# Performance work log

Hardware: AMD Instinct MI355X
Metric: run time of the kernel (lower is better)

Reference implementation:

```python
import jax, jax.numpy as jnp
import numpy as np

R, MAXI, MAXO = 333, 119, 12   # n ROIs, max roi input size, max roi reduced size
E, H = 3328, 8                  # embed dim (concat 3325 + pad 3), heads
HD = E // H                     # 416
CONCAT = 3325
EPS = 1e-5


def _roi_layout():
    """Deterministic synthetic ROI sizes + gather maps for vectorized ragged encode."""
    sizes = 30 + (7 * np.arange(R)) % 90            # per-ROI input widths
    reduced = 8 + np.arange(R) % 5                  # per-ROI output widths
    reduced[332] = 8                                # makes concat+3 divisible by 8
    starts = np.concatenate([[0], np.cumsum(sizes)[:-1]])
    total = int(sizes.sum())                        # 24696
    in_idx = np.minimum(starts[:, None] + np.arange(MAXI)[None, :], total - 1)
    in_mask = (np.arange(MAXI)[None, :] < sizes[:, None]).astype(np.float32)
    out_idx = np.concatenate([i * MAXO + np.arange(reduced[i]) for i in range(R)])
    assert out_idx.shape[0] == CONCAT
    return jnp.asarray(in_idx), jnp.asarray(in_mask), jnp.asarray(out_idx)


def _bn(x, g, b):
    # training-mode BatchNorm1d: biased batch stats (matches torch normalization)
    m = x.mean(0)
    v = x.var(0)
    return (x - m) * jax.lax.rsqrt(v + EPS) * g + b


def _lrelu(x, s):
    return jnp.where(x > 0, x, s * x)


def setup_inputs() -> dict:
    key = jax.random.key(0)
    ks = jax.random.split(key, 16)
    B, TOTAL = 2048, 24696
    f32 = jnp.float32
    return {
        'x': jax.random.normal(ks[0], (B, TOTAL), f32),
        'enc_W': jax.random.normal(ks[1], (R, MAXO, MAXI), f32) * 0.1,
        'enc_b': jax.random.normal(ks[2], (R, MAXO), f32) * 0.02,
        'bn1_g': jnp.ones((CONCAT,), f32),
        'bn1_b': jnp.zeros((CONCAT,), f32),
        'Wqkv': jax.random.normal(ks[3], (3 * E, E), f32) * (1.0 / np.sqrt(E)),
        'bqkv': jnp.zeros((3 * E,), f32),
        'Wo': jax.random.normal(ks[4], (E, E), f32) * (1.0 / np.sqrt(E)),
        'bo': jnp.zeros((E,), f32),
        'W1': jax.random.normal(ks[5], (1024, E), f32) * (1.0 / np.sqrt(E)),
        'b1': jnp.zeros((1024,), f32),
        'bn2_g': jnp.ones((1024,), f32),
        'bn2_b': jnp.zeros((1024,), f32),
        'W2': jax.random.normal(ks[6], (300, 1024), f32) * (1.0 / 32.0),
        'b2': jnp.zeros((300,), f32),
        'Wc': jax.random.normal(ks[7], (180, 300), f32) * 0.06,
        'bc': jnp.zeros((180,), f32),
    }


def reference(x, enc_W, enc_b, bn1_g, bn1_b, Wqkv, bqkv, Wo, bo,
              W1, b1, bn2_g, bn2_b, W2, b2, Wc, bc):
    in_idx, in_mask, out_idx = _roi_layout()
    B = x.shape[0]
    # --- vectorized ragged per-ROI Linear (replaces 333-way python loop) ---
    xp = x[:, in_idx] * in_mask                     # [B, R, MAXI], padded slices
    y = jnp.einsum('bri,roi->bro', xp, enc_W) + enc_b  # [B, R, MAXO]
    y = y.reshape(B, R * MAXO)[:, out_idx]          # ragged concat -> [B, 3325]
    # per-ROI BN+LeakyReLU(0.3) == per-feature on the concat
    y = _lrelu(_bn(y, bn1_g, bn1_b), 0.3)
    y = jnp.pad(y, ((0, 0), (1, 2)))                # F.pad (1, 2) -> [B, 3328]
    # --- MultiheadAttention, seq_len = 1 (input unsqueezed to [1, B, E]) ---
    qkv = y @ Wqkv.T + bqkv                         # [B, 3E]
    q, k, v = jnp.split(qkv, 3, axis=-1)
    q = q.reshape(B, H, 1, HD)
    k = k.reshape(B, H, 1, HD)
    v = v.reshape(B, H, 1, HD)
    s = jnp.einsum('bhqd,bhkd->bhqk', q, k) / jnp.sqrt(jnp.float32(HD))
    a = jax.nn.softmax(s, axis=-1)                  # trivially 1 for L=1, kept faithful
    o = jnp.einsum('bhqk,bhkd->bhqd', a, v).reshape(B, E)
    o = o @ Wo.T + bo
    r = _lrelu(_bn(o @ W1.T + b1, bn2_g, bn2_b), 0.1)
    reg_out = r @ W2.T + b2                         # [B, 300]
    y_pred = jax.nn.softmax(reg_out @ Wc.T + bc, axis=-1)  # [B, 180]
    return reg_out, y_pred
```

## Files before the change

kernel.cpp:

```cpp
#include <hip/hip_runtime.h>
#include <hip/hip_bf16.h>

#define B_      2048
#define R_      333
#define MAXI_   119
#define MAXO_   12
#define CONCAT_ 3325
#define E_      3328
#define TOTAL_  24696
#define HID_    1024
#define NREG_   300
#define NCLS_   180
#define EPS_    1e-5f
#define NSLOT_  128
#define PSTR_   3328
#define NS2_    128

typedef __attribute__((ext_vector_type(8))) short bf16x8;
typedef __attribute__((ext_vector_type(4))) float f32x4;

static __device__ inline unsigned short f2bf_rne(float f) {
  unsigned u;
  __builtin_memcpy(&u, &f, 4);
  u += 0x7fff + ((u >> 16) & 1);
  return (unsigned short)(u >> 16);
}
static __device__ inline float bf2f(unsigned short s) {
  unsigned u = (unsigned)s << 16;
  float f;
  __builtin_memcpy(&f, &u, 4);
  return f;
}

__global__ void layout_kernel(int* __restrict__ starts, int* __restrict__ red_starts) {
  if (threadIdx.x == 0 && blockIdx.x == 0) {
    int s = 0, rs = 0;
    for (int r = 0; r < R_; ++r) {
      starts[r] = s;
      red_starts[r] = rs;
      s += 30 + (7 * r) % 90;
      rs += (r == 332) ? 8 : (8 + r % 5);
    }
  }
}

__global__ __launch_bounds__(256) void prep_cast_kernel(
    const float* __restrict__ W1, unsigned short* __restrict__ W1b,
    const float* __restrict__ W2, unsigned short* __restrict__ W2b) {
  const int n4a = HID_ * E_ / 4, n4b = NREG_ * HID_ / 4;
  int i = blockIdx.x * 256 + threadIdx.x;
  const float* src; unsigned short* dst; int idx;
  if (i < n4a) { src = W1; dst = W1b; idx = i; }
  else if (i < n4a + n4b) { src = W2; dst = W2b; idx = i - n4a; }
  else return;
  float4 v = ((const float4*)src)[idx];
  ushort4 o;
  o.x = f2bf_rne(v.x); o.y = f2bf_rne(v.y); o.z = f2bf_rne(v.z); o.w = f2bf_rne(v.w);
  ((ushort4*)dst)[idx] = o;
}

__device__ __forceinline__ void rowdot_body(
    const float* __restrict__ A, const float* __restrict__ v, const float* __restrict__ b,
    float* __restrict__ out, int N, int K, int jb) {
  int wid = threadIdx.x >> 6, lane = threadIdx.x & 63;
  int j = jb * 4 + wid;
  if (j >= N) return;
  const float* row = A + (size_t)j * K;
  float s = 0.f;
  for (int k = lane; k < K; k += 64) s = fmaf(row[k], v[k], s);
  for (int o = 32; o; o >>= 1) s += __shfl_down(s, o);
  if (lane == 0) out[j] = s + b[j];
}

__global__ __launch_bounds__(256) void trans_rowdot_kernel(
    const float* __restrict__ Wo, const float* __restrict__ Wv,
    unsigned short* __restrict__ WoT, unsigned short* __restrict__ WvT,
    const float* __restrict__ bv, const float* __restrict__ bo, float* __restrict__ t1v) {
  __shared__ float tile[64][65];
  int bid = blockIdx.x;
  const int NT = (E_ / 64) * (E_ / 64);
  if (bid < 2 * NT) {
    int z = bid / NT, rem = bid % NT;
    const float* in = z ? Wv : Wo;
    unsigned short* out = z ? WvT : WoT;
    int c0 = (rem % 52) * 64, r0 = (rem / 52) * 64;
    int t = threadIdx.x;
    int ci = t & 63, ri0 = t >> 6;
    for (int ri = ri0; ri < 64; ri += 4)
      tile[ri][ci] = in[(size_t)(r0 + ri) * E_ + c0 + ci];
    __syncthreads();
    int rj = t & 63, i0 = t >> 6;
    for (int i = i0; i < 64; i += 4)
      out[(size_t)(c0 + i) * E_ + r0 + rj] = f2bf_rne(tile[rj][i]);
  } else {
    rowdot_body(Wo, bv, bo, t1v, E_, E_, bid - 2 * NT);
  }
}

__device__ __forceinline__ void pack_w_body(const float* __restrict__ enc_W,
                                            const int* __restrict__ starts,
                                            unsigned short* __restrict__ Wpk, int r) {
  int tid = threadIdx.x;
  int kc = tid >> 6, lane = tid & 63;
  int size = 30 + (7 * r) % 90;
  int s8 = starts[r] & 7;
  int oc = lane & 15;
  int k0 = kc * 32 + (lane >> 4) * 8;
  unsigned short o[8];
#pragma unroll
  for (int e = 0; e < 8; ++e) {
    int k = k0 + e - s8;
    float v = 0.f;
    if (oc < MAXO_ && k >= 0 && k < size) v = enc_W[((size_t)r * MAXO_ + oc) * MAXI_ + k];
    o[e] = f2bf_rne(v);
  }
  unsigned short* dst = Wpk + ((size_t)r * 4 + kc) * 512 + lane * 8;
  *(ushort4*)dst = *(ushort4*)&o[0];
  *(ushort4*)(dst + 4) = *(ushort4*)&o[4];
}

__global__ __launch_bounds__(256) void packw_rowdot_kernel(
    const float* __restrict__ enc_W, const int* __restrict__ starts,
    unsigned short* __restrict__ Wpk,
    const float* __restrict__ W1, const float* __restrict__ t1v,
    const float* __restrict__ b1, float* __restrict__ zbv) {
  int bid = blockIdx.x;
  if (bid < R_) pack_w_body(enc_W, starts, Wpk, bid);
  else          rowdot_body(W1, t1v, b1, zbv, HID_, E_, bid - R_);
}

__device__ __forceinline__ void encode_body(
    const float* __restrict__ x, const unsigned short* __restrict__ Wpk,
    const float* __restrict__ enc_b, const int* __restrict__ starts,
    const int* __restrict__ red_starts,
    unsigned short* __restrict__ yT, float* __restrict__ pS1, float* __restrict__ pS2,
    int r, int bg) {
  int tid = threadIdx.x;
  int wid = tid >> 6, lane = tid & 63;
  int lr = lane & 15, kg = lane >> 4;

  int size = 30 + (7 * r) % 90;
  int red  = (r == 332) ? 8 : (8 + r % 5);
  int st   = starts[r];
  int s8   = st & 7;
  int a0   = st & ~7;
  int rs   = red_starts[r];
  int nkc  = (s8 + size + 31) >> 5;
  int kmax = TOTAL_ - a0;

  bf16x8 wf[4];
  const unsigned short* wp = Wpk + (size_t)r * 2048 + lane * 8;
#pragma unroll
  for (int kc = 0; kc < 4; ++kc) wf[kc] = *(const bf16x8*)(wp + kc * 512);

  float bofs[4];
#pragma unroll
  for (int reg = 0; reg < 4; ++reg) {
    int oc = kg * 4 + reg;
    bofs[reg] = (oc < MAXO_) ? enc_b[r * MAXO_ + oc] : 0.f;
  }

  for (int t = 0; t < 4; ++t) {
    int b0 = bg * 256 + wid * 64 + t * 16;
    const float* xrow = x + (size_t)(b0 + lr) * TOTAL_ + a0;
    f32x4 acc = {0.f, 0.f, 0.f, 0.f};
#pragma unroll
    for (int kc = 0; kc < 4; ++kc) {
      if (kc < nkc) {
        int k0 = kc * 32 + kg * 8;
        if (k0 + 8 > kmax) k0 = kmax - 8;
        float4 v0 = *(const float4*)(xrow + k0);
        float4 v1 = *(const float4*)(xrow + k0 + 4);
        bf16x8 xf;
        xf[0] = (short)f2bf_rne(v0.x); xf[1] = (short)f2bf_rne(v0.y);
        xf[2] = (short)f2bf_rne(v0.z); xf[3] = (short)f2bf_rne(v0.w);
        xf[4] = (short)f2bf_rne(v1.x); xf[5] = (short)f2bf_rne(v1.y);
        xf[6] = (short)f2bf_rne(v1.z); xf[7] = (short)f2bf_rne(v1.w);
        acc = __builtin_amdgcn_mfma_f32_16x16x32_bf16(wf[kc], xf, acc, 0, 0, 0);
      }
    }
    int slot = b0 >> 4;
#pragma unroll
    for (int reg = 0; reg < 4; ++reg) {
      int oc = kg * 4 + reg;
      if (oc < red) {
        float v = acc[reg] + bofs[reg];
        yT[(size_t)(rs + oc) * B_ + b0 + lr] = f2bf_rne(v);
        float a = v, s2 = v * v;
#pragma unroll
        for (int m = 1; m <= 8; m <<= 1) { a += __shfl_xor(a, m); s2 += __shfl_xor(s2, m); }
        if (lr == 0) {
          pS1[slot * PSTR_ + rs + oc] = a;
          pS2[slot * PSTR_ + rs + oc] = s2;
        }
      }
    }
  }
}

template <int KS, bool OUT_BF16>
__device__ __forceinline__ void gemm_body(
    const unsigned short* __restrict__ A, const unsigned short* __restrict__ W,
    const float* __restrict__ bias, float* __restrict__ Cf, unsigned short* __restrict__ Cb,
    int M, int N, int K, int bx, int by, int bz,
    unsigned short* a_lds, unsigned short* b_lds) {
  int tid = threadIdx.x;
  int wid = tid >> 6, lane = tid & 63;
  int wr = wid >> 1, wc = wid & 1;
  int row0 = by * 128, col0 = bx * 64;
  int lr = lane & 15, kg = lane >> 4;
  int Klocal = K / KS;
  int kbase = bz * Klocal;

  int srow = tid >> 2, sk = (tid & 3) * 8;
  const unsigned short* aptr0 = A + (size_t)(row0 + srow) * K + kbase + sk;
  const unsigned short* aptr1 = aptr0 + (size_t)64 * K;
  int bcol = col0 + srow; if (bcol > N - 1) bcol = N - 1;
  const unsigned short* bptr = W + (size_t)bcol * K + kbase + sk;

  f32x4 acc[4][2] = {};
  int nk = Klocal >> 5;

#define STAGE_(buf, kc)                                                                             \
  do {                                                                                              \
    __builtin_amdgcn_global_load_lds((const __attribute__((address_space(1))) void*)(aptr0 + (kc)), \
        (__attribute__((address_space(3))) void*)(a_lds + (buf) * 4096 + wid * 512), 16, 0, 0);     \
    __builtin_amdgcn_global_load_lds((const __attribute__((address_space(1))) void*)(aptr1 + (kc)), \
        (__attribute__((address_space(3))) void*)(a_lds + (buf) * 4096 + 2048 + wid * 512), 16, 0, 0); \
    __builtin_amdgcn_global_load_lds((const __attribute__((address_space(1))) void*)(bptr + (kc)),  \
        (__attribute__((address_space(3))) void*)(b_lds + (buf) * 2048 + wid * 512), 16, 0, 0);     \
  } while (0)

  STAGE_(0, 0);
  __syncthreads();
  int cur = 0;
  for (int t = 0; t < nk; ++t) {
    if (t + 1 < nk) STAGE_(cur ^ 1, (t + 1) * 32);
    bf16x8 a[4], b[2];
#pragma unroll
    for (int f = 0; f < 4; ++f)
      a[f] = *(const bf16x8*)(a_lds + cur * 4096 + (wr * 64 + f * 16 + lr) * 32 + kg * 8);
#pragma unroll
    for (int f = 0; f < 2; ++f)
      b[f] = *(const bf16x8*)(b_lds + cur * 2048 + (wc * 32 + f * 16 + lr) * 32 + kg * 8);
#pragma unroll
    for (int i = 0; i < 4; ++i)
#pragma unroll
      for (int j = 0; j < 2; ++j)
        acc[i][j] = __builtin_amdgcn_mfma_f32_16x16x32_bf16(a[i], b[j], acc[i][j], 0, 0, 0);
    __syncthreads();
    cur ^= 1;
  }
#undef STAGE_

#pragma unroll
  for (int j = 0; j < 2; ++j) {
    int ccol = col0 + wc * 32 + j * 16 + lr;
    if (ccol >= N) continue;
    float bv = (KS == 1 && bias) ? bias[ccol] : 0.f;
#pragma unroll
    for (int i = 0; i < 4; ++i) {
#pragma unroll
      for (int reg = 0; reg < 4; ++reg) {
        int crow = row0 + wr * 64 + i * 16 + kg * 4 + reg;
        float v = acc[i][j][reg] + bv;
        if (KS == 1) {
          if (OUT_BF16) Cb[(size_t)crow * N + ccol] = f2bf_rne(v);
          else          Cf[(size_t)crow * N + ccol] = v;
        } else {
          Cf[((size_t)bz * M + crow) * N + ccol] = v;
        }
      }
    }
  }
}

#define ENC_NB_ (R_ * 8)
#define WA_NB_  ((E_ / 64) * (HID_ / 128))
__global__ __launch_bounds__(256) void enc_wa_kernel(
    const float* __restrict__ x, const unsigned short* __restrict__ Wpk,
    const float* __restrict__ enc_b, const int* __restrict__ starts,
    const int* __restrict__ red_starts,
    unsigned short* __restrict__ yT, float* __restrict__ pS1, float* __restrict__ pS2,
    const unsigned short* __restrict__ W1b, const unsigned short* __restrict__ WoT,
    unsigned short* __restrict__ Wa_bf) {
  __shared__ __align__(16) unsigned short smem[12288];
  int bid = blockIdx.x;
  if (bid < WA_NB_) {
    gemm_body<1, true>(W1b, WoT, nullptr, nullptr, Wa_bf, HID_, E_, E_,
                       bid % 52, bid / 52, 0, smem, smem + 8192);
  } else {
    int eb = bid - WA_NB_;
    encode_body(x, Wpk, enc_b, starts, red_starts, yT, pS1, pS2, eb >> 3, eb & 7);
  }
}

__global__ __launch_bounds__(256) void bn1_stats_kernel(const float* __restrict__ pS1,
                                                        const float* __restrict__ pS2,
                                                        float* __restrict__ mean, float* __restrict__ rstd) {
  int c = blockIdx.x * 256 + threadIdx.x;
  if (c >= CONCAT_) return;
  float s = 0.f, s2 = 0.f;
  for (int i = 0; i < NSLOT_; ++i) { s += pS1[i * PSTR_ + c]; s2 += pS2[i * PSTR_ + c]; }
  float m = s / B_;
  float v = s2 / B_ - m * m;
  mean[c] = m;
  rstd[c] = rsqrtf(v + EPS_);
}

#define TR_NB_ ((E_ / 64) * (B_ / 64))
#define WB_NB_ ((E_ / 64) * (HID_ / 128) * 2)
__global__ __launch_bounds__(256) void trans_wb_kernel(
    const unsigned short* __restrict__ yT, const float* __restrict__ mean,
    const float* __restrict__ rstd, const float* __restrict__ g,
    const float* __restrict__ bb, unsigned short* __restrict__ Y,
    const unsigned short* __restrict__ Wa_bf, const unsigned short* __restrict__ WvT,
    float* __restrict__ Cpart) {
  __shared__ __align__(16) unsigned short smem[12288];
  int bid = blockIdx.x;
  if (bid < WB_NB_) {
    gemm_body<2, false>(Wa_bf, WvT, nullptr, Cpart, nullptr, HID_, E_, E_,
                        bid % 52, (bid / 52) & 7, bid / 416, smem, smem + 8192);
  } else {
    int tb = bid - WB_NB_;
    int cc0 = (tb % 52) * 64, b0 = (tb / 52) * 64;
    float (*tile)[65] = (float(*)[65])smem;
    int t = threadIdx.x;
    int bi = t & 63, ci0 = t >> 6;
    for (int ci = ci0; ci < 64; ci += 4) {
      int c = cc0 + ci - 1;
      float v = 0.f;
      if (c >= 0 && c < CONCAT_) {
        float f = bf2f(yT[(size_t)c * B_ + b0 + bi]);
        v = (f - mean[c]) * rstd[c] * g[c] + bb[c];
        v = v > 0.f ? v : 0.3f * v;
      }
      tile[ci][bi] = v;
    }
    __syncthreads();
    int cj = t & 63, bj0 = t >> 6;
    for (int bj = bj0; bj < 64; bj += 4)
      Y[(size_t)(b0 + bj) * E_ + cc0 + cj] = f2bf_rne(tile[cj][bj]);
  }
}

__global__ __launch_bounds__(256) void combine_wb_kernel(const float* __restrict__ part,
                                                         unsigned short* __restrict__ out) {
  const int MN = HID_ * E_;
  int i = blockIdx.x * 256 + threadIdx.x;
  if (i >= MN) return;
  out[i] = f2bf_rne(part[i] + part[(size_t)MN + i]);
}

template <int KS, bool OUT_BF16>
__global__ __launch_bounds__(256) void gemm_kernel(
    const unsigned short* __restrict__ A, const unsigned short* __restrict__ W,
    const float* __restrict__ bias, float* __restrict__ Cf, unsigned short* __restrict__ Cb,
    int M, int N, int K) {
  __shared__ __align__(16) unsigned short smem[12288];
  gemm_body<KS, OUT_BF16>(A, W, bias, Cf, Cb, M, N, K,
                          blockIdx.x, blockIdx.y, blockIdx.z, smem, smem + 8192);
}

__global__ __launch_bounds__(256) void combZ_stats_kernel(
    const float* __restrict__ Cpart, const float* __restrict__ zb,
    float* __restrict__ Z, float* __restrict__ pS, float* __restrict__ pS2) {
  int c = blockIdx.x * 256 + threadIdx.x;
  int ry = blockIdx.y;
  float zbc = zb[c];
  float s1 = 0.f, s2 = 0.f;
  for (int r = ry * 16; r < ry * 16 + 16; ++r) {
    float v = zbc;
#pragma unroll
    for (int z = 0; z < 4; ++z) v += Cpart[((size_t)z * B_ + r) * HID_ + c];
    Z[(size_t)r * HID_ + c] = v;
    s1 += v; s2 = fmaf(v, v, s2);
  }
  pS[ry * HID_ + c] = s1;
  pS2[ry * HID_ + c] = s2;
}

__global__ __launch_bounds__(256) void colstats_final_kernel(
    const float* __restrict__ pS, const float* __restrict__ pS2,
    float* __restrict__ mean, float* __restrict__ rstd) {
  int c = blockIdx.x * 256 + threadIdx.x;
  if (c >= HID_) return;
  float s = 0.f, s2 = 0.f;
  for (int i = 0; i < NS2_; ++i) { s += pS[i * HID_ + c]; s2 += pS2[i * HID_ + c]; }
  float m = s / B_;
  float v = s2 / B_ - m * m;
  mean[c] = m;
  rstd[c] = rsqrtf(v + EPS_);
}

__global__ __launch_bounds__(256) void bn2_apply_kernel(
    const float* __restrict__ Z, const float* __restrict__ mean, const float* __restrict__ rstd,
    const float* __restrict__ g, const float* __restrict__ bb, unsigned short* __restrict__ R) {
  int i = blockIdx.x * 256 + threadIdx.x;
  int c = i & (HID_ - 1);
  float v = (Z[i] - mean[c]) * rstd[c] * g[c] + bb[c];
  v = v > 0.f ? v : 0.1f * v;
  R[i] = f2bf_rne(v);
}

__global__ __launch_bounds__(256) void classifier_kernel(
    const float* __restrict__ Cpart, const float* __restrict__ b2,
    const float* __restrict__ Wc, const float* __restrict__ bc,
    float* __restrict__ reg_out, float* __restrict__ ypred) {
  int b = blockIdx.x;
  __shared__ __align__(16) float rrow[NREG_];
  __shared__ float sl[256];
  int tid = threadIdx.x;
  for (int i = tid; i < NREG_; i += 256) {
    float s = b2[i];
#pragma unroll
    for (int z = 0; z < 4; ++z) s += Cpart[((size_t)z * B_ + b) * NREG_ + i];
    rrow[i] = s;
    reg_out[(size_t)b * NREG_ + i] = s;
  }
  __syncthreads();
  float s = -1e30f;
  if (tid < NCLS_) {
    const float* w = Wc + (size_t)tid * NREG_;
    float acc = 0.f;
    for (int k = 0; k < NREG_; k += 4) {
      float4 wv = *(const float4*)(w + k);
      float4 rv = *(const float4*)(&rrow[k]);
      acc = fmaf(wv.x, rv.x, acc); acc = fmaf(wv.y, rv.y, acc);
      acc = fmaf(wv.z, rv.z, acc); acc = fmaf(wv.w, rv.w, acc);
    }
    s = acc + bc[tid];
  }
  sl[tid] = s;
  __syncthreads();
  for (int o = 128; o > 0; o >>= 1) {
    if (tid < o) sl[tid] = fmaxf(sl[tid], sl[tid + o]);
    __syncthreads();
  }
  float mx = sl[0];
  __syncthreads();
  float e = (tid < NCLS_) ? __expf(s - mx) : 0.f;
  sl[tid] = e;
  __syncthreads();
  for (int o = 128; o > 0; o >>= 1) {
    if (tid < o) sl[tid] += sl[tid + o];
    __syncthreads();
  }
  if (tid < NCLS_) ypred[(size_t)b * NCLS_ + tid] = e / sl[0];
}

extern "C" void kernel_launch(void* const* d_in, const int* in_sizes, int n_in,
                              void* d_out, int out_size, void* d_ws, size_t ws_size,
                              hipStream_t stream) {
  const float* x     = (const float*)d_in[0];
  const float* enc_W = (const float*)d_in[1];
  const float* enc_b = (const float*)d_in[2];
  const float* bn1_g = (const float*)d_in[3];
  const float* bn1_b = (const float*)d_in[4];
  const float* Wqkv  = (const float*)d_in[5];
  const float* bqkv  = (const float*)d_in[6];
  const float* Wo    = (const float*)d_in[7];
  const float* bo    = (const float*)d_in[8];
  const float* W1    = (const float*)d_in[9];
  const float* b1    = (const float*)d_in[10];
  const float* bn2_g = (const float*)d_in[11];
  const float* bn2_b = (const float*)d_in[12];
  const float* W2    = (const float*)d_in[13];
  const float* b2    = (const float*)d_in[14];
  const float* Wc    = (const float*)d_in[15];
  const float* bc    = (const float*)d_in[16];

  char* ws = (char*)d_ws;
  size_t off = 0;
  auto alloc = [&](size_t bytes) -> void* {
    void* p = ws + off;
    off += (bytes + 255) & ~(size_t)255;
    return p;
  };

  unsigned short* yT     = (unsigned short*)alloc((size_t)CONCAT_ * B_ * 2);
  float*          pS1b   = (float*)alloc((size_t)NSLOT_ * PSTR_ * 4);
  float*          pS2b   = (float*)alloc((size_t)NSLOT_ * PSTR_ * 4);
  float*          mean1  = (float*)alloc(CONCAT_ * 4);
  float*          rstd1  = (float*)alloc(CONCAT_ * 4);
  unsigned short* Ybf    = (unsigned short*)alloc((size_t)B_ * E_ * 2);
  unsigned short* Rbf    = (unsigned short*)alloc((size_t)B_ * HID_ * 2);
  unsigned short* WoT_bf = (unsigned short*)alloc((size_t)E_ * E_ * 2);
  unsigned short* WvT_bf = (unsigned short*)alloc((size_t)E_ * E_ * 2);
  unsigned short* W1_bf  = (unsigned short*)alloc((size_t)HID_ * E_ * 2);
  unsigned short* W2_bf  = (unsigned short*)alloc((size_t)NREG_ * HID_ * 2);
  unsigned short* Wa_bf  = (unsigned short*)alloc((size_t)HID_ * E_ * 2);
  unsigned short* Wb_bf  = (unsigned short*)alloc((size_t)HID_ * E_ * 2);
  unsigned short* Wpk    = (unsigned short*)alloc((size_t)R_ * 2048 * 2);
  float*          Cpart  = (float*)alloc((size_t)4 * B_ * HID_ * 4);
  float*          t1v    = (float*)alloc(E_ * 4);
  float*          zbv    = (float*)alloc(HID_ * 4);
  float*          partS  = (float*)alloc((size_t)NS2_ * HID_ * 4);
  float*          partS2 = (float*)alloc((size_t)NS2_ * HID_ * 4);
  float*          mean2  = (float*)alloc(HID_ * 4);
  float*          rstd2  = (float*)alloc(HID_ * 4);
  int*            starts = (int*)alloc(R_ * 4);
  int*            redst  = (int*)alloc(R_ * 4);

  float* Z = (float*)yT;

  layout_kernel<<<1, 1, 0, stream>>>(starts, redst);
  {
    int nb = (HID_ * E_ / 4 + NREG_ * HID_ / 4 + 255) / 256;
    prep_cast_kernel<<<nb, 256, 0, stream>>>(W1, W1_bf, W2, W2_bf);
  }
  trans_rowdot_kernel<<<2 * 2704 + E_ / 4, 256, 0, stream>>>(
      Wo, Wqkv + (size_t)2 * E_ * E_, WoT_bf, WvT_bf, bqkv + 2 * E_, bo, t1v);
  packw_rowdot_kernel<<<R_ + HID_ / 4, 256, 0, stream>>>(
      enc_W, starts, Wpk, W1, t1v, b1, zbv);
  enc_wa_kernel<<<WA_NB_ + ENC_NB_, 256, 0, stream>>>(
      x, Wpk, enc_b, starts, redst, yT, pS1b, pS2b, W1_bf, WoT_bf, Wa_bf);
  bn1_stats_kernel<<<(CONCAT_ + 255) / 256, 256, 0, stream>>>(pS1b, pS2b, mean1, rstd1);
  trans_wb_kernel<<<WB_NB_ + TR_NB_, 256, 0, stream>>>(
      yT, mean1, rstd1, bn1_g, bn1_b, Ybf, Wa_bf, WvT_bf, Cpart);
  combine_wb_kernel<<<(HID_ * E_ + 255) / 256, 256, 0, stream>>>(Cpart, Wb_bf);
  gemm_kernel<4, false><<<dim3(HID_ / 64, B_ / 128, 4), 256, 0, stream>>>(
      Ybf, Wb_bf, nullptr, Cpart, nullptr, B_, HID_, E_);
  combZ_stats_kernel<<<dim3(HID_ / 256, NS2_), 256, 0, stream>>>(Cpart, zbv, Z, partS, partS2);
  colstats_final_kernel<<<(HID_ + 255) / 256, 256, 0, stream>>>(partS, partS2, mean2, rstd2);
  bn2_apply_kernel<<<(B_ * HID_) / 256, 256, 0, stream>>>(Z, mean2, rstd2, bn2_g, bn2_b, Rbf);
  gemm_kernel<4, false><<<dim3((NREG_ + 63) / 64, B_ / 128, 4), 256, 0, stream>>>(
      Rbf, W2_bf, nullptr, Cpart, nullptr, B_, NREG_, HID_);
  float* reg_out = (float*)d_out;
  classifier_kernel<<<B_, 256, 0, stream>>>(
      Cpart, b2, Wc, bc, reg_out, reg_out + (size_t)B_ * NREG_);
}
```

Before: 360.4 us.

## Widen GEMM tiles to 128x128, fuse prep kernels, double-batch encode loads

The shared GEMM body moves from a 128x64 to a 128x128 output tile, with 16 MFMA accumulators per wave and a larger LDS buffer, to improve operand reuse. The three weight-prep launches become one prep kernel, and the W1 rowdot moves into the encode/Wa kernel, cutting launches and dependency gaps. The encode loop now loads two 16-row batches of x up front before converting and issuing MFMAs, to expose more memory-level parallelism. Larger tiles mean fewer blocks (e.g. the N=300 GEMM pads to 384), and more registers may lower occupancy.

```diff
diff --git a/kernel.cpp b/kernel.cpp
--- a/kernel.cpp
+++ b/kernel.cpp
@@ -44,21 +44,6 @@
   }
 }
 
-__global__ __launch_bounds__(256) void prep_cast_kernel(
-    const float* __restrict__ W1, unsigned short* __restrict__ W1b,
-    const float* __restrict__ W2, unsigned short* __restrict__ W2b) {
-  const int n4a = HID_ * E_ / 4, n4b = NREG_ * HID_ / 4;
-  int i = blockIdx.x * 256 + threadIdx.x;
-  const float* src; unsigned short* dst; int idx;
-  if (i < n4a) { src = W1; dst = W1b; idx = i; }
-  else if (i < n4a + n4b) { src = W2; dst = W2b; idx = i - n4a; }
-  else return;
-  float4 v = ((const float4*)src)[idx];
-  ushort4 o;
-  o.x = f2bf_rne(v.x); o.y = f2bf_rne(v.y); o.z = f2bf_rne(v.z); o.w = f2bf_rne(v.w);
-  ((ushort4*)dst)[idx] = o;
-}
-
 __device__ __forceinline__ void rowdot_body(
     const float* __restrict__ A, const float* __restrict__ v, const float* __restrict__ b,
     float* __restrict__ out, int N, int K, int jb) {
@@ -72,15 +57,44 @@
   if (lane == 0) out[j] = s + b[j];
 }
 
-__global__ __launch_bounds__(256) void trans_rowdot_kernel(
+__device__ __forceinline__ void pack_w_body(const float* __restrict__ enc_W,
+                                            const int* __restrict__ starts,
+                                            unsigned short* __restrict__ Wpk, int r) {
+  int tid = threadIdx.x;
+  int kc = tid >> 6, lane = tid & 63;
+  int size = 30 + (7 * r) % 90;
+  int s8 = starts[r] & 7;
+  int oc = lane & 15;
+  int k0 = kc * 32 + (lane >> 4) * 8;
+  unsigned short o[8];
+#pragma unroll
+  for (int e = 0; e < 8; ++e) {
+    int k = k0 + e - s8;
+    float v = 0.f;
+    if (oc < MAXO_ && k >= 0 && k < size) v = enc_W[((size_t)r * MAXO_ + oc) * MAXI_ + k];
+    o[e] = f2bf_rne(v);
+  }
+  unsigned short* dst = Wpk + ((size_t)r * 4 + kc) * 512 + lane * 8;
+  *(ushort4*)dst = *(ushort4*)&o[0];
+  *(ushort4*)(dst + 4) = *(ushort4*)&o[4];
+}
+
+#define NTR_   ((E_ / 64) * (E_ / 64))
+#define NC4A_  (HID_ * E_ / 4)
+#define NC4B_  (NREG_ * HID_ / 4)
+#define NCAST_ ((NC4A_ + NC4B_ + 255) / 256)
+__global__ __launch_bounds__(256) void prep_kernel(
     const float* __restrict__ Wo, const float* __restrict__ Wv,
     unsigned short* __restrict__ WoT, unsigned short* __restrict__ WvT,
-    const float* __restrict__ bv, const float* __restrict__ bo, float* __restrict__ t1v) {
+    const float* __restrict__ W1, unsigned short* __restrict__ W1b,
+    const float* __restrict__ W2, unsigned short* __restrict__ W2b,
+    const float* __restrict__ bv, const float* __restrict__ bo, float* __restrict__ t1v,
+    const float* __restrict__ enc_W, const int* __restrict__ starts,
+    unsigned short* __restrict__ Wpk) {
   __shared__ float tile[64][65];
   int bid = blockIdx.x;
-  const int NT = (E_ / 64) * (E_ / 64);
-  if (bid < 2 * NT) {
-    int z = bid / NT, rem = bid % NT;
+  if (bid < 2 * NTR_) {
+    int z = bid / NTR_, rem = bid % NTR_;
     const float* in = z ? Wv : Wo;
     unsigned short* out = z ? WvT : WoT;
     int c0 = (rem % 52) * 64, r0 = (rem / 52) * 64;
@@ -92,41 +106,21 @@
     int rj = t & 63, i0 = t >> 6;
     for (int i = i0; i < 64; i += 4)
       out[(size_t)(c0 + i) * E_ + r0 + rj] = f2bf_rne(tile[rj][i]);
+  } else if (bid < 2 * NTR_ + NCAST_) {
+    int i = (bid - 2 * NTR_) * 256 + threadIdx.x;
+    const float* src; unsigned short* dst; int idx;
+    if (i < NC4A_) { src = W1; dst = W1b; idx = i; }
+    else if (i < NC4A_ + NC4B_) { src = W2; dst = W2b; idx = i - NC4A_; }
+    else return;
+    float4 v = ((const float4*)src)[idx];
+    ushort4 o;
+    o.x = f2bf_rne(v.x); o.y = f2bf_rne(v.y); o.z = f2bf_rne(v.z); o.w = f2bf_rne(v.w);
+    ((ushort4*)dst)[idx] = o;
+  } else if (bid < 2 * NTR_ + NCAST_ + E_ / 4) {
+    rowdot_body(Wo, bv, bo, t1v, E_, E_, bid - 2 * NTR_ - NCAST_);
   } else {
-    rowdot_body(Wo, bv, bo, t1v, E_, E_, bid - 2 * NT);
-  }
-}
-
-__device__ __forceinline__ void pack_w_body(const float* __restrict__ enc_W,
-                                            const int* __restrict__ starts,
-                                            unsigned short* __restrict__ Wpk, int r) {
-  int tid = threadIdx.x;
-  int kc = tid >> 6, lane = tid & 63;
-  int size = 30 + (7 * r) % 90;
-  int s8 = starts[r] & 7;
-  int oc = lane & 15;
-  int k0 = kc * 32 + (lane >> 4) * 8;
-  unsigned short o[8];
-#pragma unroll
-  for (int e = 0; e < 8; ++e) {
-    int k = k0 + e - s8;
-    float v = 0.f;
-    if (oc < MAXO_ && k >= 0 && k < size) v = enc_W[((size_t)r * MAXO_ + oc) * MAXI_ + k];
-    o[e] = f2bf_rne(v);
-  }
-  unsigned short* dst = Wpk + ((size_t)r * 4 + kc) * 512 + lane * 8;
-  *(ushort4*)dst = *(ushort4*)&o[0];
-  *(ushort4*)(dst + 4) = *(ushort4*)&o[4];
-}
-
-__global__ __launch_bounds__(256) void packw_rowdot_kernel(
-    const float* __restrict__ enc_W, const int* __restrict__ starts,
-    unsigned short* __restrict__ Wpk,
-    const float* __restrict__ W1, const float* __restrict__ t1v,
-    const float* __restrict__ b1, float* __restrict__ zbv) {
-  int bid = blockIdx.x;
-  if (bid < R_) pack_w_body(enc_W, starts, Wpk, bid);
-  else          rowdot_body(W1, t1v, b1, zbv, HID_, E_, bid - R_);
+    pack_w_body(enc_W, starts, Wpk, bid - 2 * NTR_ - NCAST_ - E_ / 4);
+  }
 }
 
 __device__ __forceinline__ void encode_body(
@@ -160,38 +154,63 @@
     bofs[reg] = (oc < MAXO_) ? enc_b[r * MAXO_ + oc] : 0.f;
   }
 
-  for (int t = 0; t < 4; ++t) {
-    int b0 = bg * 256 + wid * 64 + t * 16;
-    const float* xrow = x + (size_t)(b0 + lr) * TOTAL_ + a0;
-    f32x4 acc = {0.f, 0.f, 0.f, 0.f};
+  int ks[4];
+#pragma unroll
+  for (int kc = 0; kc < 4; ++kc) {
+    int k0 = kc * 32 + kg * 8;
+    if (k0 + 8 > kmax) k0 = kmax - 8;
+    ks[kc] = k0;
+  }
+
+  for (int tp = 0; tp < 2; ++tp) {
+    int b0a = bg * 256 + wid * 64 + tp * 32;
+    int b0b = b0a + 16;
+    const float* xra = x + (size_t)(b0a + lr) * TOTAL_ + a0;
+    const float* xrb = x + (size_t)(b0b + lr) * TOTAL_ + a0;
+    float4 va[4][2], vb[4][2];
 #pragma unroll
     for (int kc = 0; kc < 4; ++kc) {
       if (kc < nkc) {
-        int k0 = kc * 32 + kg * 8;
-        if (k0 + 8 > kmax) k0 = kmax - 8;
-        float4 v0 = *(const float4*)(xrow + k0);
-        float4 v1 = *(const float4*)(xrow + k0 + 4);
-        bf16x8 xf;
-        xf[0] = (short)f2bf_rne(v0.x); xf[1] = (short)f2bf_rne(v0.y);
-        xf[2] = (short)f2bf_rne(v0.z); xf[3] = (short)f2bf_rne(v0.w);
-        xf[4] = (short)f2bf_rne(v1.x); xf[5] = (short)f2bf_rne(v1.y);
-        xf[6] = (short)f2bf_rne(v1.z); xf[7] = (short)f2bf_rne(v1.w);
-        acc = __builtin_amdgcn_mfma_f32_16x16x32_bf16(wf[kc], xf, acc, 0, 0, 0);
+        va[kc][0] = *(const float4*)(xra + ks[kc]);
+        va[kc][1] = *(const float4*)(xra + ks[kc] + 4);
+        vb[kc][0] = *(const float4*)(xrb + ks[kc]);
+        vb[kc][1] = *(const float4*)(xrb + ks[kc] + 4);
       }
     }
-    int slot = b0 >> 4;
-#pragma unroll
-    for (int reg = 0; reg < 4; ++reg) {
-      int oc = kg * 4 + reg;
-      if (oc < red) {
-        float v = acc[reg] + bofs[reg];
-        yT[(size_t)(rs + oc) * B_ + b0 + lr] = f2bf_rne(v);
-        float a = v, s2 = v * v;
-#pragma unroll
-        for (int m = 1; m <= 8; m <<= 1) { a += __shfl_xor(a, m); s2 += __shfl_xor(s2, m); }
-        if (lr == 0) {
-          pS1[slot * PSTR_ + rs + oc] = a;
-          pS2[slot * PSTR_ + rs + oc] = s2;
+    f32x4 acca = {0.f, 0.f, 0.f, 0.f}, accb = {0.f, 0.f, 0.f, 0.f};
+#pragma unroll
+    for (int kc = 0; kc < 4; ++kc) {
+      if (kc < nkc) {
+        bf16x8 xfa, xfb;
+#pragma unroll
+        for (int e = 0; e < 4; ++e) {
+          xfa[e]     = (short)f2bf_rne(va[kc][0][e]);
+          xfa[e + 4] = (short)f2bf_rne(va[kc][1][e]);
+          xfb[e]     = (short)f2bf_rne(vb[kc][0][e]);
+          xfb[e + 4] = (short)f2bf_rne(vb[kc][1][e]);
+        }
+        acca = __builtin_amdgcn_mfma_f32_16x16x32_bf16(wf[kc], xfa, acca, 0, 0, 0);
+        accb = __builtin_amdgcn_mfma_f32_16x16x32_bf16(wf[kc], xfb, accb, 0, 0, 0);
+      }
+    }
+#pragma unroll
+    for (int half = 0; half < 2; ++half) {
+      int b0 = half ? b0b : b0a;
+      f32x4 acc = half ? accb : acca;
+      int slot = b0 >> 4;
+#pragma unroll
+      for (int reg = 0; reg < 4; ++reg) {
+        int oc = kg * 4 + reg;
+        if (oc < red) {
+          float v = acc[reg] + bofs[reg];
+          yT[(size_t)(rs + oc) * B_ + b0 + lr] = f2bf_rne(v);
+          float a = v, s2 = v * v;
+#pragma unroll
+          for (int m = 1; m <= 8; m <<= 1) { a += __shfl_xor(a, m); s2 += __shfl_xor(s2, m); }
+          if (lr == 0) {
+            pS1[slot * PSTR_ + rs + oc] = a;
+            pS2[slot * PSTR_ + rs + oc] = s2;
+          }
         }
       }
     }
@@ -201,13 +220,14 @@
 template <int KS, bool OUT_BF16>
 __device__ __forceinline__ void gemm_body(
     const unsigned short* __restrict__ A, const unsigned short* __restrict__ W,
-    const float* __restrict__ bias, float* __restrict__ Cf, unsigned short* __restrict__ Cb,
-    int M, int N, int K, int bx, int by, int bz,
-    unsigned short* a_lds, unsigned short* b_lds) {
+    float* __restrict__ Cf, unsigned short* __restrict__ Cb,
+    int M, int N, int K, int bx, int by, int bz, unsigned short* smem) {
+  unsigned short* a_lds = smem;
+  unsigned short* b_lds = smem + 8192;
   int tid = threadIdx.x;
   int wid = tid >> 6, lane = tid & 63;
   int wr = wid >> 1, wc = wid & 1;
-  int row0 = by * 128, col0 = bx * 64;
+  int row0 = by * 128, col0 = bx * 128;
   int lr = lane & 15, kg = lane >> 4;
   int Klocal = K / KS;
   int kbase = bz * Klocal;
@@ -215,10 +235,12 @@
   int srow = tid >> 2, sk = (tid & 3) * 8;
   const unsigned short* aptr0 = A + (size_t)(row0 + srow) * K + kbase + sk;
   const unsigned short* aptr1 = aptr0 + (size_t)64 * K;
-  int bcol = col0 + srow; if (bcol > N - 1) bcol = N - 1;
-  const unsigned short* bptr = W + (size_t)bcol * K + kbase + sk;
-
-  f32x4 acc[4][2] = {};
+  int bcol0 = col0 + srow;      if (bcol0 > N - 1) bcol0 = N - 1;
+  int bcol1 = col0 + 64 + srow; if (bcol1 > N - 1) bcol1 = N - 1;
+  const unsigned short* bptr0 = W + (size_t)bcol0 * K + kbase + sk;
+  const unsigned short* bptr1 = W + (size_t)bcol1 * K + kbase + sk;
+
+  f32x4 acc[4][4] = {};
   int nk = Klocal >> 5;
 
 #define STAGE_(buf, kc)                                                                             \
@@ -227,8 +249,10 @@
         (__attribute__((address_space(3))) void*)(a_lds + (buf) * 4096 + wid * 512), 16, 0, 0);     \
     __builtin_amdgcn_global_load_lds((const __attribute__((address_space(1))) void*)(aptr1 + (kc)), \
         (__attribute__((address_space(3))) void*)(a_lds + (buf) * 4096 + 2048 + wid * 512), 16, 0, 0); \
-    __builtin_amdgcn_global_load_lds((const __attribute__((address_space(1))) void*)(bptr + (kc)),  \
-        (__attribute__((address_space(3))) void*)(b_lds + (buf) * 2048 + wid * 512), 16, 0, 0);     \
+    __builtin_amdgcn_global_load_lds((const __attribute__((address_space(1))) void*)(bptr0 + (kc)), \
+        (__attribute__((address_space(3))) void*)(b_lds + (buf) * 4096 + wid * 512), 16, 0, 0);     \
+    __builtin_amdgcn_global_load_lds((const __attribute__((address_space(1))) void*)(bptr1 + (kc)), \
+        (__attribute__((address_space(3))) void*)(b_lds + (buf) * 4096 + 2048 + wid * 512), 16, 0, 0); \
   } while (0)
 
   STAGE_(0, 0);
@@ -236,17 +260,16 @@
   int cur = 0;
   for (int t = 0; t < nk; ++t) {
     if (t + 1 < nk) STAGE_(cur ^ 1, (t + 1) * 32);
-    bf16x8 a[4], b[2];
-#pragma unroll
-    for (int f = 0; f < 4; ++f)
+    bf16x8 a[4], b[4];
+#pragma unroll
+    for (int f = 0; f < 4; ++f) {
       a[f] = *(const bf16x8*)(a_lds + cur * 4096 + (wr * 64 + f * 16 + lr) * 32 + kg * 8);
-#pragma unroll
-    for (int f = 0; f < 2; ++f)
-      b[f] = *(const bf16x8*)(b_lds + cur * 2048 + (wc * 32 + f * 16 + lr) * 32 + kg * 8);
+      b[f] = *(const bf16x8*)(b_lds + cur * 4096 + (wc * 64 + f * 16 + lr) * 32 + kg * 8);
+    }
 #pragma unroll
     for (int i = 0; i < 4; ++i)
 #pragma unroll
-      for (int j = 0; j < 2; ++j)
+      for (int j = 0; j < 4; ++j)
         acc[i][j] = __builtin_amdgcn_mfma_f32_16x16x32_bf16(a[i], b[j], acc[i][j], 0, 0, 0);
     __syncthreads();
     cur ^= 1;
@@ -254,16 +277,15 @@
 #undef STAGE_
 
 #pragma unroll
-  for (int j = 0; j < 2; ++j) {
-    int ccol = col0 + wc * 32 + j * 16 + lr;
+  for (int j = 0; j < 4; ++j) {
+    int ccol = col0 + wc * 64 + j * 16 + lr;
     if (ccol >= N) continue;
-    float bv = (KS == 1 && bias) ? bias[ccol] : 0.f;
 #pragma unroll
     for (int i = 0; i < 4; ++i) {
 #pragma unroll
       for (int reg = 0; reg < 4; ++reg) {
         int crow = row0 + wr * 64 + i * 16 + kg * 4 + reg;
-        float v = acc[i][j][reg] + bv;
+        float v = acc[i][j][reg];
         if (KS == 1) {
           if (OUT_BF16) Cb[(size_t)crow * N + ccol] = f2bf_rne(v);
           else          Cf[(size_t)crow * N + ccol] = v;
@@ -275,23 +297,27 @@
   }
 }
 
+#define WA_NB_  ((E_ / 128) * (HID_ / 128))
 #define ENC_NB_ (R_ * 8)
-#define WA_NB_  ((E_ / 64) * (HID_ / 128))
 __global__ __launch_bounds__(256) void enc_wa_kernel(
     const float* __restrict__ x, const unsigned short* __restrict__ Wpk,
     const float* __restrict__ enc_b, const int* __restrict__ starts,
     const int* __restrict__ red_starts,
     unsigned short* __restrict__ yT, float* __restrict__ pS1, float* __restrict__ pS2,
     const unsigned short* __restrict__ W1b, const unsigned short* __restrict__ WoT,
-    unsigned short* __restrict__ Wa_bf) {
-  __shared__ __align__(16) unsigned short smem[12288];
+    unsigned short* __restrict__ Wa_bf,
+    const float* __restrict__ W1, const float* __restrict__ t1v,
+    const float* __restrict__ b1, float* __restrict__ zbv) {
+  __shared__ __align__(16) unsigned short smem[16384];
   int bid = blockIdx.x;
   if (bid < WA_NB_) {
-    gemm_body<1, true>(W1b, WoT, nullptr, nullptr, Wa_bf, HID_, E_, E_,
-                       bid % 52, bid / 52, 0, smem, smem + 8192);
-  } else {
+    gemm_body<1, true>(W1b, WoT, nullptr, Wa_bf, HID_, E_, E_,
+                       bid % (E_ / 128), bid / (E_ / 128), 0, smem);
+  } else if (bid < WA_NB_ + ENC_NB_) {
     int eb = bid - WA_NB_;
     encode_body(x, Wpk, enc_b, starts, red_starts, yT, pS1, pS2, eb >> 3, eb & 7);
+  } else {
+    rowdot_body(W1, t1v, b1, zbv, HID_, E_, bid - WA_NB_ - ENC_NB_);
   }
 }
 
@@ -308,19 +334,20 @@
   rstd[c] = rsqrtf(v + EPS_);
 }
 
+#define WB_NB_ ((E_ / 128) * (HID_ / 128) * 2)
 #define TR_NB_ ((E_ / 64) * (B_ / 64))
-#define WB_NB_ ((E_ / 64) * (HID_ / 128) * 2)
 __global__ __launch_bounds__(256) void trans_wb_kernel(
     const unsigned short* __restrict__ yT, const float* __restrict__ mean,
     const float* __restrict__ rstd, const float* __restrict__ g,
     const float* __restrict__ bb, unsigned short* __restrict__ Y,
     const unsigned short* __restrict__ Wa_bf, const unsigned short* __restrict__ WvT,
     float* __restrict__ Cpart) {
-  __shared__ __align__(16) unsigned short smem[12288];
+  __shared__ __align__(16) unsigned short smem[16384];
   int bid = blockIdx.x;
   if (bid < WB_NB_) {
-    gemm_body<2, false>(Wa_bf, WvT, nullptr, Cpart, nullptr, HID_, E_, E_,
-                        bid % 52, (bid / 52) & 7, bid / 416, smem, smem + 8192);
+    int z = bid / (WB_NB_ / 2), rem = bid % (WB_NB_ / 2);
+    gemm_body<2, false>(Wa_bf, WvT, Cpart, nullptr, HID_, E_, E_,
+                        rem % (E_ / 128), rem / (E_ / 128), z, smem);
   } else {
     int tb = bid - WB_NB_;
     int cc0 = (tb % 52) * 64, b0 = (tb / 52) * 64;
@@ -355,11 +382,9 @@
 template <int KS, bool OUT_BF16>
 __global__ __launch_bounds__(256) void gemm_kernel(
     const unsigned short* __restrict__ A, const unsigned short* __restrict__ W,
-    const float* __restrict__ bias, float* __restrict__ Cf, unsigned short* __restrict__ Cb,
-    int M, int N, int K) {
-  __shared__ __align__(16) unsigned short smem[12288];
-  gemm_body<KS, OUT_BF16>(A, W, bias, Cf, Cb, M, N, K,
-                          blockIdx.x, blockIdx.y, blockIdx.z, smem, smem + 8192);
+    float* __restrict__ Cf, unsigned short* __restrict__ Cb, int M, int N, int K) {
+  __shared__ __align__(16) unsigned short smem[16384];
+  gemm_body<KS, OUT_BF16>(A, W, Cf, Cb, M, N, K, blockIdx.x, blockIdx.y, blockIdx.z, smem);
 }
 
 __global__ __launch_bounds__(256) void combZ_stats_kernel(
@@ -505,27 +530,22 @@
   float* Z = (float*)yT;
 
   layout_kernel<<<1, 1, 0, stream>>>(starts, redst);
-  {
-    int nb = (HID_ * E_ / 4 + NREG_ * HID_ / 4 + 255) / 256;
-    prep_cast_kernel<<<nb, 256, 0, stream>>>(W1, W1_bf, W2, W2_bf);
-  }
-  trans_rowdot_kernel<<<2 * 2704 + E_ / 4, 256, 0, stream>>>(
-      Wo, Wqkv + (size_t)2 * E_ * E_, WoT_bf, WvT_bf, bqkv + 2 * E_, bo, t1v);
-  packw_rowdot_kernel<<<R_ + HID_ / 4, 256, 0, stream>>>(
-      enc_W, starts, Wpk, W1, t1v, b1, zbv);
-  enc_wa_kernel<<<WA_NB_ + ENC_NB_, 256, 0, stream>>>(
-      x, Wpk, enc_b, starts, redst, yT, pS1b, pS2b, W1_bf, WoT_bf, Wa_bf);
+  prep_kernel<<<2 * NTR_ + NCAST_ + E_ / 4 + R_, 256, 0, stream>>>(
+      Wo, Wqkv + (size_t)2 * E_ * E_, WoT_bf, WvT_bf,
+      W1, W1_bf, W2, W2_bf, bqkv + 2 * E_, bo, t1v, enc_W, starts, Wpk);
+  enc_wa_kernel<<<WA_NB_ + ENC_NB_ + HID_ / 4, 256, 0, stream>>>(
+      x, Wpk, enc_b, starts, redst, yT, pS1b, pS2b, W1_bf, WoT_bf, Wa_bf, W1, t1v, b1, zbv);
   bn1_stats_kernel<<<(CONCAT_ + 255) / 256, 256, 0, stream>>>(pS1b, pS2b, mean1, rstd1);
   trans_wb_kernel<<<WB_NB_ + TR_NB_, 256, 0, stream>>>(
       yT, mean1, rstd1, bn1_g, bn1_b, Ybf, Wa_bf, WvT_bf, Cpart);
   combine_wb_kernel<<<(HID_ * E_ + 255) / 256, 256, 0, stream>>>(Cpart, Wb_bf);
-  gemm_kernel<4, false><<<dim3(HID_ / 64, B_ / 128, 4), 256, 0, stream>>>(
-      Ybf, Wb_bf, nullptr, Cpart, nullptr, B_, HID_, E_);
+  gemm_kernel<4, false><<<dim3(HID_ / 128, B_ / 128, 4), 256, 0, stream>>>(
+      Ybf, Wb_bf, Cpart, nullptr, B_, HID_, E_);
   combZ_stats_kernel<<<dim3(HID_ / 256, NS2_), 256, 0, stream>>>(Cpart, zbv, Z, partS, partS2);
   colstats_final_kernel<<<(HID_ + 255) / 256, 256, 0, stream>>>(partS, partS2, mean2, rstd2);
   bn2_apply_kernel<<<(B_ * HID_) / 256, 256, 0, stream>>>(Z, mean2, rstd2, bn2_g, bn2_b, Rbf);
-  gemm_kernel<4, false><<<dim3((NREG_ + 63) / 64, B_ / 128, 4), 256, 0, stream>>>(
-      Rbf, W2_bf, nullptr, Cpart, nullptr, B_, NREG_, HID_);
+  gemm_kernel<4, false><<<dim3((NREG_ + 127) / 128, B_ / 128, 4), 256, 0, stream>>>(
+      Rbf, W2_bf, Cpart, nullptr, B_, NREG_, HID_);
   float* reg_out = (float*)d_out;
   classifier_kernel<<<B_, 256, 0, stream>>>(
       Cpart, b2, Wc, bc, reg_out, reg_out + (size_t)B_ * NREG_);
```

Result: faster. 336.9 us (-6.5%).
